# Kernel tuning notes

Measured on AMD Instinct MI355X. Metric: run time of the kernel, lower is better.

## Reference

```python
import jax, jax.numpy as jnp
import numpy as np

B, T, INP, E, H, N = 16, 256, 1536, 512, 8, 16
D = E // H            # 64, must equal default dim_head for to_out shapes to work
SCALE = D ** -0.5
EPS = 1e-5


def _ln(x, g, b):
    m = x.mean(-1, keepdims=True)
    v = ((x - m) ** 2).mean(-1, keepdims=True)
    return (x - m) * jax.lax.rsqrt(v + EPS) * g + b


def _attend(q, k, v, Wo, bo):
    # q,k,v: [bt, h, n, d]. NOTE: attend is LogSoftmax, not Softmax (faithful).
    dots = jnp.einsum('bhnd,bhmd->bhnm', q, k) * SCALE
    a = jax.nn.log_softmax(dots, axis=-1)
    o = jnp.einsum('bhnm,bhmd->bhnd', a, v)
    o = o.transpose(0, 2, 1, 3).reshape(o.shape[0], N, E)  # b n (h d)
    return o @ Wo + bo


def _self_attn(x, Wqkv, Wo, bo):
    # x is already LayerNormed (PreNorm); residual adds the normed x (faithful).
    qkv = x @ Wqkv  # [bt, n, 3E]
    q, k, v = jnp.split(qkv, 3, axis=-1)
    hd = lambda t: t.reshape(t.shape[0], N, H, D).transpose(0, 2, 1, 3)
    return _attend(hd(q), hd(k), hd(v), Wo, bo) + x


def _ff(x, W1, b1, W2, b2):
    # x already LayerNormed; residual adds normed x (faithful to PreNorm+FF).
    return jax.nn.gelu(x @ W1 + b1, approximate=False) @ W2 + b2 + x


def setup_inputs() -> dict:
    key = jax.random.key(0)
    ks = iter(jax.random.split(key, 64))
    nrm = lambda shape, s=0.02: jax.random.normal(next(ks), shape, jnp.float32) * s
    inp = {
        'features': jax.random.normal(next(ks), (B, T, INP), jnp.float32),
        'targets_array': jax.random.randint(next(ks), (B, T), 0, N, jnp.int64),
        'emb': nrm((N, E), 1.0),
        'Wf': nrm((INP, 2 * E * N)), 'bf': jnp.zeros((2 * E * N,), jnp.float32),
        # layer 0: Attention (tuple path: only to_out used)
        'att0_Wo': nrm((E, E)), 'att0_bo': jnp.zeros((E,), jnp.float32),
        'Wm': nrm((E, 1)), 'bm': jnp.zeros((1,), jnp.float32),
    }
    for i in range(3):
        inp[f'ff{i}_g'] = jnp.ones((E,), jnp.float32)
        inp[f'ff{i}_b'] = jnp.zeros((E,), jnp.float32)
        inp[f'ff{i}_W1'] = nrm((E, 2 * E)); inp[f'ff{i}_b1'] = jnp.zeros((2 * E,), jnp.float32)
        inp[f'ff{i}_W2'] = nrm((2 * E, E)); inp[f'ff{i}_b2'] = jnp.zeros((E,), jnp.float32)
    for i in (1, 2):
        inp[f'att{i}_g'] = jnp.ones((E,), jnp.float32)
        inp[f'att{i}_b'] = jnp.zeros((E,), jnp.float32)
        inp[f'att{i}_Wqkv'] = nrm((E, 3 * E))
        inp[f'att{i}_Wo'] = nrm((E, E)); inp[f'att{i}_bo'] = jnp.zeros((E,), jnp.float32)
    return inp


def reference(features, targets_array, emb, Wf, bf, att0_Wo, att0_bo, Wm, bm,
              ff0_g, ff0_b, ff0_W1, ff0_b1, ff0_W2, ff0_b2,
              ff1_g, ff1_b, ff1_W1, ff1_b1, ff1_W2, ff1_b2,
              ff2_g, ff2_b, ff2_W1, ff2_b1, ff2_W2, ff2_b2,
              att1_g, att1_b, att1_Wqkv, att1_Wo, att1_bo,
              att2_g, att2_b, att2_Wqkv, att2_Wo, att2_bo):
    f = features.reshape(-1, INP)                 # [BT, INP]
    t = targets_array.reshape(-1)                 # [BT]
    kv = f @ Wf + bf                              # [BT, 2*E*N]
    k_, v_ = jnp.split(kv, 2, axis=-1)
    nhd = lambda x: x.reshape(-1, N, H, D).transpose(0, 2, 1, 3)  # b (n h d) -> b h n d
    k, v = nhd(k_), nhd(v_)
    q = emb[t].reshape(-1, H, 1, D)               # b h d -> b h 1 d
    q = jnp.broadcast_to(q, (q.shape[0], H, N, D))
    # layer stack: Attn(tuple), PreNorm(FF), PreNorm(Attn), PreNorm(FF), PreNorm(Attn), PreNorm(FF)
    x = _attend(q, k, v, att0_Wo, att0_bo)        # [BT, N, E]
    x = _ff(_ln(x, ff0_g, ff0_b), ff0_W1, ff0_b1, ff0_W2, ff0_b2)
    x = _self_attn(_ln(x, att1_g, att1_b), att1_Wqkv, att1_Wo, att1_bo)
    x = _ff(_ln(x, ff1_g, ff1_b), ff1_W1, ff1_b1, ff1_W2, ff1_b2)
    x = _self_attn(_ln(x, att2_g, att2_b), att2_Wqkv, att2_Wo, att2_bo)
    x = _ff(_ln(x, ff2_g, ff2_b), ff2_W1, ff2_b1, ff2_W2, ff2_b2)
    out = x.mean(axis=1)                          # mean over targets -> [BT, E]
    out = out.reshape(B, T, E)
    mean = out @ Wm + bm                          # [B, T, 1]
    return mean
```

## Files before the change

kernel.cpp:

```cpp
#include <hip/hip_runtime.h>
#include <math.h>

#define BTOT 4096
#define INP  1536
#define EDIM 512
#define NTOK 16
#define KVW  16384
#define ENW  8192
#define FFH  1024
#define NDOT 2048

typedef __attribute__((ext_vector_type(8))) __bf16 bf16x8;
typedef __attribute__((ext_vector_type(4))) float f32x4;

__device__ __forceinline__ ushort f2bf(float f) {
    union { float f; unsigned u; } v; v.f = f;
    unsigned r = v.u + 0x7fffu + ((v.u >> 16) & 1u);
    return (ushort)(r >> 16);
}
__device__ __forceinline__ float bf2f(ushort h) {
    union { unsigned u; float f; } v; v.u = ((unsigned)h) << 16;
    return v.f;
}

__device__ __forceinline__ void transpose_body(
    const float* in, int ld, int c0, int R, ushort* out,
    int bx, int by, int tid)
{
    __shared__ float t[64][65];
    const int bc = bx * 64 + c0;
    const int br = by * 64;
#pragma unroll
    for (int it = 0; it < 16; ++it) {
        int idx = tid + it * 256;
        int r = idx >> 6, c = idx & 63;
        t[r][c] = in[(size_t)(br + r) * ld + bc + c];
    }
    __syncthreads();
    const int C0 = bx * 64;
#pragma unroll
    for (int it = 0; it < 4; ++it) {
        int idx = tid + it * 256;
        int cc = idx >> 4, rp = idx & 15;
        uint2 w2;
        w2.x = f2bf(t[4 * rp + 0][cc]) | ((unsigned)f2bf(t[4 * rp + 1][cc]) << 16);
        w2.y = f2bf(t[4 * rp + 2][cc]) | ((unsigned)f2bf(t[4 * rp + 3][cc]) << 16);
        *reinterpret_cast<uint2*>(out + (size_t)(C0 + cc) * R + br + 4 * rp) = w2;
    }
}

__global__ __launch_bounds__(256) void transpose_bf16_k(
    const float* __restrict__ in, int ld, int c0, int R,
    ushort* __restrict__ out)
{
    transpose_body(in, ld, c0, R, out, blockIdx.x, blockIdx.y, threadIdx.x);
}

struct TJob { const float* in; ushort* out; int ld, c0, R, gbx, gby; };
struct TJobs { TJob j[9]; };

__global__ __launch_bounds__(256) void transpose_batch_k(TJobs jobs)
{
    TJob jb = jobs.j[blockIdx.z];
    if ((int)blockIdx.x >= jb.gbx || (int)blockIdx.y >= jb.gby) return;
    transpose_body(jb.in, jb.ld, jb.c0, jb.R, jb.out,
                   blockIdx.x, blockIdx.y, threadIdx.x);
}

__global__ __launch_bounds__(256) void conv_bf16_k(
    const float* __restrict__ in, ushort* __restrict__ out, int n8)
{
    int i = blockIdx.x * 256 + threadIdx.x;
    if (i >= n8) return;
    const float4* p = reinterpret_cast<const float4*>(in) + 2 * (size_t)i;
    float4 a = p[0], b = p[1];
    uint4 o;
    o.x = f2bf(a.x) | ((unsigned)f2bf(a.y) << 16);
    o.y = f2bf(a.z) | ((unsigned)f2bf(a.w) << 16);
    o.z = f2bf(b.x) | ((unsigned)f2bf(b.y) << 16);
    o.w = f2bf(b.z) | ((unsigned)f2bf(b.w) << 16);
    reinterpret_cast<uint4*>(out)[i] = o;
}

__global__ __launch_bounds__(256) void conv_wv_k(
    const float* __restrict__ s0, const float* __restrict__ s1,
    ushort* __restrict__ d0, ushort* __restrict__ d1)
{
    const float* src = blockIdx.y ? s1 : s0;
    ushort* dst = blockIdx.y ? d1 : d0;
    int idx = blockIdx.x * 256 + threadIdx.x;
    int row = idx >> 6, c8 = (idx & 63) * 8;
    const float4* p = reinterpret_cast<const float4*>(
        src + (size_t)row * (3 * EDIM) + 2 * EDIM + c8);
    float4 a = p[0], b = p[1];
    uint4 o;
    o.x = f2bf(a.x) | ((unsigned)f2bf(a.y) << 16);
    o.y = f2bf(a.z) | ((unsigned)f2bf(a.w) << 16);
    o.z = f2bf(b.x) | ((unsigned)f2bf(b.y) << 16);
    o.w = f2bf(b.z) | ((unsigned)f2bf(b.w) << 16);
    *reinterpret_cast<uint4*>(dst + (size_t)row * EDIM + c8) = o;
}

__global__ __launch_bounds__(256) void gproj_k(
    const float* __restrict__ Wf, const float* __restrict__ bfv,
    const float* __restrict__ emb, ushort* __restrict__ BTg,
    float* __restrict__ C0s)
{
    const int hm = blockIdx.x;
    const int h = hm >> 4, m = hm & 15;
    const int l = threadIdx.x & 63, w = threadIdx.x >> 6;
    const int t = l & 15, isub = l >> 4;
    const int colb = m * 512 + h * 64;
    const int ibase = blockIdx.y * (INP / 8);

    float4 e[16];
#pragma unroll
    for (int q = 0; q < 16; ++q)
        e[q] = *reinterpret_cast<const float4*>(emb + t * EDIM + h * 64 + q * 4);

    const int n = t * 128 + hm;
    for (int i0 = ibase; i0 < ibase + INP / 8; i0 += 16) {
        const int i = i0 + w * 4 + isub;
        const float* wr = Wf + (size_t)i * KVW + colb;
        float acc = 0.f;
#pragma unroll
        for (int q = 0; q < 16; ++q) {
            float4 v4 = *reinterpret_cast<const float4*>(wr + q * 4);
            acc = fmaf(v4.x, e[q].x, fmaf(v4.y, e[q].y,
                  fmaf(v4.z, e[q].z, fmaf(v4.w, e[q].w, acc))));
        }
        BTg[(size_t)n * INP + i] = f2bf(acc);
    }
    if (blockIdx.y == 0 && w == 0 && isub == 0) {
        const float* br = bfv + colb;
        float acc = 0.f;
#pragma unroll
        for (int q = 0; q < 16; ++q) {
            float4 v4 = *reinterpret_cast<const float4*>(br + q * 4);
            acc = fmaf(v4.x, e[q].x, fmaf(v4.y, e[q].y,
                  fmaf(v4.z, e[q].z, fmaf(v4.w, e[q].w, acc))));
        }
        C0s[n] = 0.125f * acc;
    }
}

__global__ __launch_bounds__(256) void sortperm_k(
    const int* __restrict__ targets, int* __restrict__ perm,
    int* __restrict__ boff)
{
    __shared__ int cnt[NTOK], off[NTOK + 1], cur[NTOK];
    const int tid = threadIdx.x;
    if (tid < NTOK) cnt[tid] = 0;
    __syncthreads();
    for (int i = tid; i < BTOT; i += 256) atomicAdd(&cnt[targets[i]], 1);
    __syncthreads();
    if (tid == 0) {
        int s = 0;
        for (int b = 0; b < NTOK; ++b) { off[b] = s; cur[b] = s; s += cnt[b]; }
        off[NTOK] = s;
        for (int b = 0; b <= NTOK; ++b) boff[b] = off[b];
    }
    __syncthreads();
    for (int i = tid; i < BTOT; i += 256) {
        int t = targets[i];
        int p = atomicAdd(&cur[t], 1);
        perm[p] = i;
    }
}

template <int BM, int BN, int WM, int WN, int NW, bool GELU, bool OUTBF>
__global__ __launch_bounds__(NW * 64) void gemm_mfma_k(
    const ushort* __restrict__ A, int lda,
    const ushort* __restrict__ BT, int ldb,
    void* __restrict__ Cp, int ldc, int K,
    const float* __restrict__ bias,
    const float* __restrict__ res, int ldr,
    float scale)
{
    static_assert((BM / WM) * (BN / WN) == NW, "wave grid");
    static_assert(BM % (NW * 8) == 0 && BN % (NW * 8) == 0, "staging");
    constexpr int FM = WM / 16, FN = WN / 16;
    constexpr int IA = BM * 8 / (NW * 64), IB = BN * 8 / (NW * 64);
    constexpr int RA = BM / NW, RB = BN / NW;

    __shared__ bf16x8 As[BM][8];
    __shared__ bf16x8 Bs[BN][8];
    const int tid = threadIdx.x;
    const int l   = tid & 63;
    const int w   = tid >> 6;
    const int wm  = w / (BN / WN), wn = w % (BN / WN);
    const int brow = blockIdx.y * BM, bcol = blockIdx.x * BN;

    const int lr = l >> 3;
    const int ls = (l & 7) ^ lr;
    const ushort* Ab = A  + (size_t)(brow + w * RA + lr) * lda + ls * 8;
    const ushort* Bb = BT + (size_t)(bcol + w * RB + lr) * ldb + ls * 8;

    f32x4 acc[FM][FN];
#pragma unroll
    for (int i = 0; i < FM; ++i)
#pragma unroll
        for (int j = 0; j < FN; ++j) acc[i][j] = (f32x4)0.f;

    for (int k0 = 0; k0 < K; k0 += 64) {
#pragma unroll
        for (int i = 0; i < IA; ++i)
            __builtin_amdgcn_global_load_lds(
                (const __attribute__((address_space(1))) void*)(Ab + (size_t)(i * 8) * lda + k0),
                (__attribute__((address_space(3))) void*)&As[w * RA + i * 8][0],
                16, 0, 0);
#pragma unroll
        for (int i = 0; i < IB; ++i)
            __builtin_amdgcn_global_load_lds(
                (const __attribute__((address_space(1))) void*)(Bb + (size_t)(i * 8) * ldb + k0),
                (__attribute__((address_space(3))) void*)&Bs[w * RB + i * 8][0],
                16, 0, 0);
        __syncthreads();
#pragma unroll
        for (int kh = 0; kh < 2; ++kh) {
            const int slot = (kh * 4 + (l >> 4)) ^ (l & 7);
            bf16x8 af[FM], bfr[FN];
#pragma unroll
            for (int mt = 0; mt < FM; ++mt)
                af[mt] = As[wm * WM + mt * 16 + (l & 15)][slot];
#pragma unroll
            for (int nt = 0; nt < FN; ++nt)
                bfr[nt] = Bs[wn * WN + nt * 16 + (l & 15)][slot];
#pragma unroll
            for (int mt = 0; mt < FM; ++mt)
#pragma unroll
                for (int nt = 0; nt < FN; ++nt)
                    acc[mt][nt] = __builtin_amdgcn_mfma_f32_16x16x32_bf16(
                        af[mt], bfr[nt], acc[mt][nt], 0, 0, 0);
        }
        __syncthreads();
    }

    const int cr = (l >> 4) * 4, cc = l & 15;
#pragma unroll
    for (int mt = 0; mt < FM; ++mt) {
#pragma unroll
        for (int nt = 0; nt < FN; ++nt) {
            const int gc = bcol + wn * WN + nt * 16 + cc;
            const float bv = bias ? bias[gc] : 0.f;
#pragma unroll
            for (int r = 0; r < 4; ++r) {
                const size_t gr = (size_t)brow + wm * WM + mt * 16 + cr + r;
                float v = acc[mt][nt][r] * scale + bv;
                if (GELU) v = 0.5f * v * (1.f + erff(v * 0.70710678118654752f));
                if (res) v += res[gr * ldr + gc];
                if (OUTBF) ((ushort*)Cp)[gr * ldc + gc] = f2bf(v);
                else       ((float*)Cp)[gr * ldc + gc]  = v;
            }
        }
    }
}

__global__ __launch_bounds__(256) void gemm_dots_k(
    const ushort* __restrict__ A,
    const ushort* __restrict__ BT,
    const int* __restrict__ perm, const int* __restrict__ boff,
    const float* __restrict__ C0s, float* __restrict__ Csel)
{
    const int bucket = blockIdx.y;
    const int off = boff[bucket], end = boff[bucket + 1];
    const int tile = blockIdx.x;
    if (tile * 128 >= end - off) return;

    __shared__ bf16x8 As[128][8];
    __shared__ bf16x8 Bs[128][8];
    const int tid = threadIdx.x;
    const int l = tid & 63, w = tid >> 6;
    const int wm = w >> 1, wn = w & 1;
    const int lr = l >> 3;
    const int ls = (l & 7) ^ lr;

    int rowidx[4];
#pragma unroll
    for (int i = 0; i < 4; ++i) {
        int rg = off + tile * 128 + w * 32 + lr + i * 8;
        rowidx[i] = perm[rg < end ? rg : off];
    }
    const ushort* Bb = BT + (size_t)(bucket * 128 + w * 32 + lr) * INP + ls * 8;

    f32x4 acc[4][4];
#pragma unroll
    for (int i = 0; i < 4; ++i)
#pragma unroll
        for (int j = 0; j < 4; ++j) acc[i][j] = (f32x4)0.f;

    for (int k0 = 0; k0 < INP; k0 += 64) {
#pragma unroll
        for (int i = 0; i < 4; ++i)
            __builtin_amdgcn_global_load_lds(
                (const __attribute__((address_space(1))) void*)(
                    A + (size_t)rowidx[i] * INP + ls * 8 + k0),
                (__attribute__((address_space(3))) void*)&As[w * 32 + i * 8][0],
                16, 0, 0);
#pragma unroll
        for (int i = 0; i < 4; ++i)
            __builtin_amdgcn_global_load_lds(
                (const __attribute__((address_space(1))) void*)(
                    Bb + (size_t)(i * 8) * INP + k0),
                (__attribute__((address_space(3))) void*)&Bs[w * 32 + i * 8][0],
                16, 0, 0);
        __syncthreads();
#pragma unroll
        for (int kh = 0; kh < 2; ++kh) {
            const int slot = (kh * 4 + (l >> 4)) ^ (l & 7);
            bf16x8 af[4], bfr[4];
#pragma unroll
            for (int mt = 0; mt < 4; ++mt)
                af[mt] = As[wm * 64 + mt * 16 + (l & 15)][slot];
#pragma unroll
            for (int nt = 0; nt < 4; ++nt)
                bfr[nt] = Bs[wn * 64 + nt * 16 + (l & 15)][slot];
#pragma unroll
            for (int mt = 0; mt < 4; ++mt)
#pragma unroll
                for (int nt = 0; nt < 4; ++nt)
                    acc[mt][nt] = __builtin_amdgcn_mfma_f32_16x16x32_bf16(
                        af[mt], bfr[nt], acc[mt][nt], 0, 0, 0);
        }
        __syncthreads();
    }

    const int cr = (l >> 4) * 4, cc = l & 15;
#pragma unroll
    for (int mt = 0; mt < 4; ++mt) {
#pragma unroll
        for (int nt = 0; nt < 4; ++nt) {
            const int gc = wn * 64 + nt * 16 + cc;
            const float bv = C0s[bucket * 128 + gc];
#pragma unroll
            for (int r = 0; r < 4; ++r) {
                int rg = off + tile * 128 + wm * 64 + mt * 16 + cr + r;
                int orow = perm[rg < end ? rg : off];
                Csel[(size_t)orow * 128 + gc] = acc[mt][nt][r] * 0.125f + bv;
            }
        }
    }
}

__global__ __launch_bounds__(512) void attend0_k(
    const float* __restrict__ dots, const ushort* __restrict__ vb,
    ushort* __restrict__ o)
{
    const int bt = blockIdx.x;
    const int l  = threadIdx.x & 63;
    const int h  = threadIdx.x >> 6;
    const int dg = l & 7, mg = l >> 3;

    const float* dp = dots + (size_t)bt * 128 + h * 16;
    float dts[2] = {dp[mg], dp[8 + mg]};

    float mx = fmaxf(dts[0], dts[1]);
#pragma unroll
    for (int off = 8; off < 64; off <<= 1) mx = fmaxf(mx, __shfl_xor(mx, off, 64));
    float e = expf(dts[0] - mx) + expf(dts[1] - mx);
#pragma unroll
    for (int off = 8; off < 64; off <<= 1) e += __shfl_xor(e, off, 64);
    const float lse = mx + logf(e);
    const float a0 = dts[0] - lse, a1 = dts[1] - lse;

    const ushort* base = vb + (size_t)bt * ENW + h * 64 + dg * 8;
    uint4 v0 = *reinterpret_cast<const uint4*>(base + (size_t)mg * EDIM);
    uint4 v1 = *reinterpret_cast<const uint4*>(base + (size_t)(8 + mg) * EDIM);
    const ushort* u0 = reinterpret_cast<const ushort*>(&v0);
    const ushort* u1 = reinterpret_cast<const ushort*>(&v1);
    float acc[8];
#pragma unroll
    for (int j = 0; j < 8; ++j)
        acc[j] = a0 * bf2f(u0[j]) + a1 * bf2f(u1[j]);
#pragma unroll
    for (int off = 8; off < 64; off <<= 1)
#pragma unroll
        for (int j = 0; j < 8; ++j) acc[j] += __shfl_xor(acc[j], off, 64);

    if (mg == 0) {
        uint4 pk;
        pk.x = f2bf(acc[0]) | ((unsigned)f2bf(acc[1]) << 16);
        pk.y = f2bf(acc[2]) | ((unsigned)f2bf(acc[3]) << 16);
        pk.z = f2bf(acc[4]) | ((unsigned)f2bf(acc[5]) << 16);
        pk.w = f2bf(acc[6]) | ((unsigned)f2bf(acc[7]) << 16);
        *reinterpret_cast<uint4*>(o + (size_t)bt * EDIM + h * 64 + dg * 8) = pk;
    }
}

__global__ __launch_bounds__(256) void ln_k(
    const float* __restrict__ x, const float* __restrict__ g,
    const float* __restrict__ b, float* __restrict__ y,
    ushort* __restrict__ yb)
{
    const int row = blockIdx.x * 4 + (threadIdx.x >> 6);
    const int lane = threadIdx.x & 63;
    const float* xr = x + (size_t)row * EDIM + lane * 8;
    float4 a0 = *reinterpret_cast<const float4*>(xr);
    float4 a1 = *reinterpret_cast<const float4*>(xr + 4);
    float v[8] = {a0.x, a0.y, a0.z, a0.w, a1.x, a1.y, a1.z, a1.w};

    float s = 0.f;
#pragma unroll
    for (int j = 0; j < 8; ++j) s += v[j];
#pragma unroll
    for (int off = 32; off; off >>= 1) s += __shfl_xor(s, off, 64);
    const float m = s * (1.f / 512.f);

    float q = 0.f;
#pragma unroll
    for (int j = 0; j < 8; ++j) { float d = v[j] - m; q = fmaf(d, d, q); }
#pragma unroll
    for (int off = 32; off; off >>= 1) q += __shfl_xor(q, off, 64);
    const float inv = rsqrtf(q * (1.f / 512.f) + 1e-5f);

    const int c = lane * 8;
    float4 g0 = *reinterpret_cast<const float4*>(g + c);
    float4 g1 = *reinterpret_cast<const float4*>(g + c + 4);
    float4 b0 = *reinterpret_cast<const float4*>(b + c);
    float4 b1 = *reinterpret_cast<const float4*>(b + c + 4);
    float gg[8] = {g0.x, g0.y, g0.z, g0.w, g1.x, g1.y, g1.z, g1.w};
    float bb[8] = {b0.x, b0.y, b0.z, b0.w, b1.x, b1.y, b1.z, b1.w};
    float out[8];
#pragma unroll
    for (int j = 0; j < 8; ++j) out[j] = (v[j] - m) * inv * gg[j] + bb[j];
    float* yr = y + (size_t)row * EDIM + c;
    *reinterpret_cast<float4*>(yr) = make_float4(out[0], out[1], out[2], out[3]);
    *reinterpret_cast<float4*>(yr + 4) = make_float4(out[4], out[5], out[6], out[7]);
    uint4 p;
    p.x = f2bf(out[0]) | ((unsigned)f2bf(out[1]) << 16);
    p.y = f2bf(out[2]) | ((unsigned)f2bf(out[3]) << 16);
    p.z = f2bf(out[4]) | ((unsigned)f2bf(out[5]) << 16);
    p.w = f2bf(out[6]) | ((unsigned)f2bf(out[7]) << 16);
    *reinterpret_cast<uint4*>(yb + (size_t)row * EDIM + c) = p;
}

__global__ __launch_bounds__(256) void final_k(
    const float* __restrict__ x, const float* __restrict__ Wm,
    const float* __restrict__ bm, float* __restrict__ out)
{
    const int row = blockIdx.x * 4 + (threadIdx.x >> 6);
    const int lane = threadIdx.x & 63;
    const float* xr = x + (size_t)row * EDIM + lane * 8;
    const float* wr = Wm + lane * 8;
    float s = 0.f;
#pragma unroll
    for (int j = 0; j < 8; ++j) s = fmaf(xr[j], wr[j], s);
#pragma unroll
    for (int off = 32; off; off >>= 1) s += __shfl_xor(s, off, 64);
    if (lane == 0) out[row] = s + bm[0];
}

extern "C" void kernel_launch(void* const* d_in, const int* in_sizes, int n_in,
                              void* d_out, int out_size, void* d_ws, size_t ws_size,
                              hipStream_t stream)
{
    (void)in_sizes; (void)n_in; (void)out_size;
    const float* features = (const float*)d_in[0];
    const int*   targets  = (const int*)d_in[1];
    const float* emb      = (const float*)d_in[2];
    const float* Wf       = (const float*)d_in[3];
    const float* bfv      = (const float*)d_in[4];
    const float* a0Wo     = (const float*)d_in[5];
    const float* a0bo     = (const float*)d_in[6];
    const float* Wm       = (const float*)d_in[7];
    const float* bm       = (const float*)d_in[8];
    const float *ffg[3], *ffb[3], *W1[3], *b1[3], *W2[3], *b2[3];
    for (int i = 0; i < 3; ++i) {
        ffg[i] = (const float*)d_in[9 + 6 * i];
        ffb[i] = (const float*)d_in[10 + 6 * i];
        W1[i]  = (const float*)d_in[11 + 6 * i];
        b1[i]  = (const float*)d_in[12 + 6 * i];
        W2[i]  = (const float*)d_in[13 + 6 * i];
        b2[i]  = (const float*)d_in[14 + 6 * i];
    }
    const float *ag[2], *abp[2], *aWqkv[2], *aWo[2], *abo[2];
    for (int i = 0; i < 2; ++i) {
        ag[i]    = (const float*)d_in[27 + 5 * i];
        abp[i]   = (const float*)d_in[28 + 5 * i];
        aWqkv[i] = (const float*)d_in[29 + 5 * i];
        aWo[i]   = (const float*)d_in[30 + 5 * i];
        abo[i]   = (const float*)d_in[31 + 5 * i];
    }

    char* wsc = (char*)d_ws;
    auto alloc = [&](size_t bytes) { char* p = wsc; wsc += bytes; return p; };
    ushort* WfvT  = (ushort*)alloc((size_t)ENW * INP * 2);
    ushort* BTg   = (ushort*)alloc((size_t)NDOT * INP * 2);
    float*  C0s   = (float*) alloc((size_t)NDOT * 4);
    float*  dsel  = (float*) alloc((size_t)BTOT * 128 * 4);
    int*    perm  = (int*)   alloc((size_t)BTOT * 4);
    int*    boff  = (int*)   alloc(32 * 4);
    ushort* a0WoT = (ushort*)alloc((size_t)EDIM * EDIM * 2);
    ushort *W1T[3], *W2T[3], *WoT[2], *Wv_bf[2], *WcombT[2];
    for (int i = 0; i < 3; ++i) {
        W1T[i] = (ushort*)alloc((size_t)FFH * EDIM * 2);
        W2T[i] = (ushort*)alloc((size_t)EDIM * FFH * 2);
    }
    for (int i = 0; i < 2; ++i) {
        WoT[i]    = (ushort*)alloc((size_t)EDIM * EDIM * 2);
        Wv_bf[i]  = (ushort*)alloc((size_t)EDIM * EDIM * 2);
        WcombT[i] = (ushort*)alloc((size_t)EDIM * EDIM * 2);
    }
    ushort* featb = (ushort*)alloc((size_t)BTOT * INP * 2);
    ushort* o_b   = (ushort*)alloc((size_t)BTOT * EDIM * 2);
    float*  x     = (float*) alloc((size_t)BTOT * EDIM * 4);
    float*  xln   = (float*) alloc((size_t)BTOT * EDIM * 4);
    ushort* xlnb  = (ushort*)alloc((size_t)BTOT * EDIM * 2);
    ushort* hb    = (ushort*)alloc((size_t)BTOT * FFH * 2);
    const size_t fixed = (size_t)(wsc - (char*)d_ws);
    int CB = BTOT;
    while (CB > 256 && fixed + (size_t)CB * ENW * 2 > ws_size) CB >>= 1;
    ushort* vb = (ushort*)alloc((size_t)CB * ENW * 2);

    const dim3 blk(256, 1, 1);

    conv_bf16_k<<<(BTOT * INP / 8 + 255) / 256, blk, 0, stream>>>(
        features, featb, BTOT * INP / 8);
    gproj_k<<<dim3(128, 8), blk, 0, stream>>>(Wf, bfv, emb, BTg, C0s);
    sortperm_k<<<1, blk, 0, stream>>>(targets, perm, boff);
    transpose_bf16_k<<<dim3(ENW / 64, INP / 64), blk, 0, stream>>>(
        Wf, KVW, ENW, INP, WfvT);

    TJobs tj;
    tj.j[0] = {a0Wo, a0WoT, EDIM, 0, EDIM, 8, 8};
    for (int i = 0; i < 3; ++i) {
        tj.j[1 + 2 * i] = {W1[i], W1T[i], FFH, 0, EDIM, 16, 8};
        tj.j[2 + 2 * i] = {W2[i], W2T[i], EDIM, 0, FFH, 8, 16};
    }
    tj.j[7] = {aWo[0], WoT[0], EDIM, 0, EDIM, 8, 8};
    tj.j[8] = {aWo[1], WoT[1], EDIM, 0, EDIM, 8, 8};
    transpose_batch_k<<<dim3(16, 16, 9), blk, 0, stream>>>(tj);

    conv_wv_k<<<dim3(128, 2), blk, 0, stream>>>(aWqkv[0], aWqkv[1],
                                                Wv_bf[0], Wv_bf[1]);

    const float CATT = -44.36141955583650f;
    for (int i = 0; i < 2; ++i)
        gemm_mfma_k<64, 128, 32, 64, 4, false, true>
            <<<dim3(EDIM / 128, EDIM / 64), blk, 0, stream>>>(
            WoT[i], EDIM, Wv_bf[i], EDIM, WcombT[i], EDIM, EDIM,
            nullptr, nullptr, 0, CATT);

    gemm_dots_k<<<dim3(32, 16), blk, 0, stream>>>(featb, BTg, perm, boff,
                                                  C0s, dsel);
    for (int c0 = 0; c0 < BTOT; c0 += CB) {
        gemm_mfma_k<128, 128, 64, 64, 4, false, true>
            <<<dim3(ENW / 128, CB / 128), blk, 0, stream>>>(
            featb + (size_t)c0 * INP, INP, WfvT, INP, vb, ENW, INP,
            bfv + ENW, nullptr, 0, 1.f);
        attend0_k<<<CB, 512, 0, stream>>>(dsel + (size_t)c0 * 128, vb,
                                          o_b + (size_t)c0 * EDIM);
    }
    gemm_mfma_k<64, 128, 32, 64, 4, false, false>
        <<<dim3(EDIM / 128, BTOT / 64), blk, 0, stream>>>(
        o_b, EDIM, a0WoT, EDIM, x, EDIM, EDIM, a0bo, nullptr, 0, 1.f);

    auto ln = [&](const float* g, const float* b) {
        ln_k<<<BTOT / 4, blk, 0, stream>>>(x, g, b, xln, xlnb);
    };
    auto ff = [&](int i) {
        ln(ffg[i], ffb[i]);
        gemm_mfma_k<64, 128, 32, 64, 4, true, true>
            <<<dim3(FFH / 128, BTOT / 64), blk, 0, stream>>>(
            xlnb, EDIM, W1T[i], EDIM, hb, FFH, EDIM, b1[i], nullptr, 0, 1.f);
        gemm_mfma_k<64, 128, 32, 64, 4, false, false>
            <<<dim3(EDIM / 128, BTOT / 64), blk, 0, stream>>>(
            hb, FFH, W2T[i], FFH, x, EDIM, FFH, b2[i], xln, EDIM, 1.f);
    };
    auto attn = [&](int i) {
        ln(ag[i], abp[i]);
        gemm_mfma_k<64, 128, 32, 64, 4, false, false>
            <<<dim3(EDIM / 128, BTOT / 64), blk, 0, stream>>>(
            xlnb, EDIM, WcombT[i], EDIM, x, EDIM, EDIM, abo[i], xln, EDIM, 1.f);
    };

    ff(0);
    attn(0);
    ff(1);
    attn(1);
    ff(2);

    final_k<<<BTOT / 4, blk, 0, stream>>>(x, Wm, bm, (float*)d_out);
}
```

Measured before the change: 493.7 us.

## Fuse V projection with layer-0 attention weighting and move log-softmax into dots epilogue

The big V projection GEMM now writes no 4096x8192 bf16 intermediate. The Wf value columns are transposed into a permuted layout so each 128-column tile holds all 16 tokens for a few head dims. The new GEMM epilogue then multiplies by the log-softmax weights and reduces across tokens with shuffles, writing the attention output directly. Log-softmax moves into the dots GEMM epilogue, and sortperm is folded into the gproj launch as an extra block row. This removes a large HBM round trip and several launches, at the cost of a more complex epilogue and a single-buffered custom GEMM.

```diff
diff --git a/kernel.cpp b/kernel.cpp
--- a/kernel.cpp
+++ b/kernel.cpp
@@ -49,13 +49,6 @@
     }
 }
 
-__global__ __launch_bounds__(256) void transpose_bf16_k(
-    const float* __restrict__ in, int ld, int c0, int R,
-    ushort* __restrict__ out)
-{
-    transpose_body(in, ld, c0, R, out, blockIdx.x, blockIdx.y, threadIdx.x);
-}
-
 struct TJob { const float* in; ushort* out; int ld, c0, R, gbx, gby; };
 struct TJobs { TJob j[9]; };
 
@@ -65,6 +58,35 @@
     if ((int)blockIdx.x >= jb.gbx || (int)blockIdx.y >= jb.gby) return;
     transpose_body(jb.in, jb.ld, jb.c0, jb.R, jb.out,
                    blockIdx.x, blockIdx.y, threadIdx.x);
+}
+
+__global__ __launch_bounds__(256) void transpose_wfvp_k(
+    const float* __restrict__ in, ushort* __restrict__ out)
+{
+    __shared__ float t[64][65];
+    const int tid = threadIdx.x;
+    const int bc = blockIdx.x * 64 + ENW;
+    const int br = blockIdx.y * 64;
+#pragma unroll
+    for (int it = 0; it < 16; ++it) {
+        int idx = tid + it * 256;
+        int r = idx >> 6, c = idx & 63;
+        t[r][c] = in[(size_t)(br + r) * KVW + bc + c];
+    }
+    __syncthreads();
+    const int C0 = blockIdx.x * 64;
+#pragma unroll
+    for (int it = 0; it < 4; ++it) {
+        int idx = tid + it * 256;
+        int cc = idx >> 4, rp = idx & 15;
+        const int n = C0 + cc;
+        const int m = n >> 9, h = (n >> 6) & 7, d8 = (n >> 3) & 7, dl = n & 7;
+        const int np = h * 1024 + d8 * 128 + dl * 16 + m;
+        uint2 w2;
+        w2.x = f2bf(t[4 * rp + 0][cc]) | ((unsigned)f2bf(t[4 * rp + 1][cc]) << 16);
+        w2.y = f2bf(t[4 * rp + 2][cc]) | ((unsigned)f2bf(t[4 * rp + 3][cc]) << 16);
+        *reinterpret_cast<uint2*>(out + (size_t)np * INP + br + 4 * rp) = w2;
+    }
 }
 
 __global__ __launch_bounds__(256) void conv_bf16_k(
@@ -104,8 +126,32 @@
 __global__ __launch_bounds__(256) void gproj_k(
     const float* __restrict__ Wf, const float* __restrict__ bfv,
     const float* __restrict__ emb, ushort* __restrict__ BTg,
-    float* __restrict__ C0s)
-{
+    float* __restrict__ C0s, const int* __restrict__ targets,
+    int* __restrict__ perm, int* __restrict__ boff)
+{
+    if (blockIdx.y == 8) {
+        if (blockIdx.x != 0) return;
+        __shared__ int cnt[NTOK], off_s[NTOK], cur[NTOK];
+        const int tid = threadIdx.x;
+        if (tid < NTOK) cnt[tid] = 0;
+        __syncthreads();
+        for (int i = tid; i < BTOT; i += 256) atomicAdd(&cnt[targets[i]], 1);
+        __syncthreads();
+        if (tid == 0) {
+            int s = 0;
+            for (int b = 0; b < NTOK; ++b) { off_s[b] = s; cur[b] = s; s += cnt[b]; }
+            for (int b = 0; b < NTOK; ++b) boff[b] = off_s[b];
+            boff[NTOK] = s;
+        }
+        __syncthreads();
+        for (int i = tid; i < BTOT; i += 256) {
+            int t = targets[i];
+            int p = atomicAdd(&cur[t], 1);
+            perm[p] = i;
+        }
+        return;
+    }
+
     const int hm = blockIdx.x;
     const int h = hm >> 4, m = hm & 15;
     const int l = threadIdx.x & 63, w = threadIdx.x >> 6;
@@ -141,30 +187,6 @@
                   fmaf(v4.z, e[q].z, fmaf(v4.w, e[q].w, acc))));
         }
         C0s[n] = 0.125f * acc;
-    }
-}
-
-__global__ __launch_bounds__(256) void sortperm_k(
-    const int* __restrict__ targets, int* __restrict__ perm,
-    int* __restrict__ boff)
-{
-    __shared__ int cnt[NTOK], off[NTOK + 1], cur[NTOK];
-    const int tid = threadIdx.x;
-    if (tid < NTOK) cnt[tid] = 0;
-    __syncthreads();
-    for (int i = tid; i < BTOT; i += 256) atomicAdd(&cnt[targets[i]], 1);
-    __syncthreads();
-    if (tid == 0) {
-        int s = 0;
-        for (int b = 0; b < NTOK; ++b) { off[b] = s; cur[b] = s; s += cnt[b]; }
-        off[NTOK] = s;
-        for (int b = 0; b <= NTOK; ++b) boff[b] = off[b];
-    }
-    __syncthreads();
-    for (int i = tid; i < BTOT; i += 256) {
-        int t = targets[i];
-        int p = atomicAdd(&cur[t], 1);
-        perm[p] = i;
     }
 }
 
@@ -334,56 +356,107 @@
             const float bv = C0s[bucket * 128 + gc];
 #pragma unroll
             for (int r = 0; r < 4; ++r) {
+                float val = acc[mt][nt][r] * 0.125f + bv;
+                float mx = val;
+                mx = fmaxf(mx, __shfl_xor(mx, 1, 64));
+                mx = fmaxf(mx, __shfl_xor(mx, 2, 64));
+                mx = fmaxf(mx, __shfl_xor(mx, 4, 64));
+                mx = fmaxf(mx, __shfl_xor(mx, 8, 64));
+                float e = expf(val - mx);
+                e += __shfl_xor(e, 1, 64);
+                e += __shfl_xor(e, 2, 64);
+                e += __shfl_xor(e, 4, 64);
+                e += __shfl_xor(e, 8, 64);
+                const float lse = mx + logf(e);
                 int rg = off + tile * 128 + wm * 64 + mt * 16 + cr + r;
                 int orow = perm[rg < end ? rg : off];
-                Csel[(size_t)orow * 128 + gc] = acc[mt][nt][r] * 0.125f + bv;
+                Csel[(size_t)orow * 128 + gc] = val - lse;
             }
         }
     }
 }
 
-__global__ __launch_bounds__(512) void attend0_k(
-    const float* __restrict__ dots, const ushort* __restrict__ vb,
+__global__ __launch_bounds__(256) void gemm_vo_k(
+    const ushort* __restrict__ A,
+    const ushort* __restrict__ BT,
+    const float* __restrict__ biasv,
+    const float* __restrict__ dsel,
     ushort* __restrict__ o)
 {
-    const int bt = blockIdx.x;
-    const int l  = threadIdx.x & 63;
-    const int h  = threadIdx.x >> 6;
-    const int dg = l & 7, mg = l >> 3;
-
-    const float* dp = dots + (size_t)bt * 128 + h * 16;
-    float dts[2] = {dp[mg], dp[8 + mg]};
-
-    float mx = fmaxf(dts[0], dts[1]);
-#pragma unroll
-    for (int off = 8; off < 64; off <<= 1) mx = fmaxf(mx, __shfl_xor(mx, off, 64));
-    float e = expf(dts[0] - mx) + expf(dts[1] - mx);
-#pragma unroll
-    for (int off = 8; off < 64; off <<= 1) e += __shfl_xor(e, off, 64);
-    const float lse = mx + logf(e);
-    const float a0 = dts[0] - lse, a1 = dts[1] - lse;
-
-    const ushort* base = vb + (size_t)bt * ENW + h * 64 + dg * 8;
-    uint4 v0 = *reinterpret_cast<const uint4*>(base + (size_t)mg * EDIM);
-    uint4 v1 = *reinterpret_cast<const uint4*>(base + (size_t)(8 + mg) * EDIM);
-    const ushort* u0 = reinterpret_cast<const ushort*>(&v0);
-    const ushort* u1 = reinterpret_cast<const ushort*>(&v1);
-    float acc[8];
-#pragma unroll
-    for (int j = 0; j < 8; ++j)
-        acc[j] = a0 * bf2f(u0[j]) + a1 * bf2f(u1[j]);
-#pragma unroll
-    for (int off = 8; off < 64; off <<= 1)
-#pragma unroll
-        for (int j = 0; j < 8; ++j) acc[j] += __shfl_xor(acc[j], off, 64);
-
-    if (mg == 0) {
-        uint4 pk;
-        pk.x = f2bf(acc[0]) | ((unsigned)f2bf(acc[1]) << 16);
-        pk.y = f2bf(acc[2]) | ((unsigned)f2bf(acc[3]) << 16);
-        pk.z = f2bf(acc[4]) | ((unsigned)f2bf(acc[5]) << 16);
-        pk.w = f2bf(acc[6]) | ((unsigned)f2bf(acc[7]) << 16);
-        *reinterpret_cast<uint4*>(o + (size_t)bt * EDIM + h * 64 + dg * 8) = pk;
+    __shared__ bf16x8 As[128][8];
+    __shared__ bf16x8 Bs[128][8];
+    const int tid = threadIdx.x;
+    const int l = tid & 63, w = tid >> 6;
+    const int wm = w >> 1, wn = w & 1;
+    const int brow = blockIdx.y * 128, bcol = blockIdx.x * 128;
+    const int h = blockIdx.x >> 3, d8 = blockIdx.x & 7;
+    const int lr = l >> 3;
+    const int ls = (l & 7) ^ lr;
+    const ushort* Ab = A  + (size_t)(brow + w * 32 + lr) * INP + ls * 8;
+    const ushort* Bb = BT + (size_t)(bcol + w * 32 + lr) * INP + ls * 8;
+
+    f32x4 acc[4][4];
+#pragma unroll
+    for (int i = 0; i < 4; ++i)
+#pragma unroll
+        for (int j = 0; j < 4; ++j) acc[i][j] = (f32x4)0.f;
+
+    for (int k0 = 0; k0 < INP; k0 += 64) {
+#pragma unroll
+        for (int i = 0; i < 4; ++i)
+            __builtin_amdgcn_global_load_lds(
+                (const __attribute__((address_space(1))) void*)(Ab + (size_t)(i * 8) * INP + k0),
+                (__attribute__((address_space(3))) void*)&As[w * 32 + i * 8][0],
+                16, 0, 0);
+#pragma unroll
+        for (int i = 0; i < 4; ++i)
+            __builtin_amdgcn_global_load_lds(
+                (const __attribute__((address_space(1))) void*)(Bb + (size_t)(i * 8) * INP + k0),
+                (__attribute__((address_space(3))) void*)&Bs[w * 32 + i * 8][0],
+                16, 0, 0);
+        __syncthreads();
+#pragma unroll
+        for (int kh = 0; kh < 2; ++kh) {
+            const int slot = (kh * 4 + (l >> 4)) ^ (l & 7);
+            bf16x8 af[4], bfr[4];
+#pragma unroll
+            for (int mt = 0; mt < 4; ++mt)
+                af[mt] = As[wm * 64 + mt * 16 + (l & 15)][slot];
+#pragma unroll
+            for (int nt = 0; nt < 4; ++nt)
+                bfr[nt] = Bs[wn * 64 + nt * 16 + (l & 15)][slot];
+#pragma unroll
+            for (int mt = 0; mt < 4; ++mt)
+#pragma unroll
+                for (int nt = 0; nt < 4; ++nt)
+                    acc[mt][nt] = __builtin_amdgcn_mfma_f32_16x16x32_bf16(
+                        af[mt], bfr[nt], acc[mt][nt], 0, 0, 0);
+        }
+        __syncthreads();
+    }
+
+    const int cr = (l >> 4) * 4, cc = l & 15;
+    float bv[4];
+#pragma unroll
+    for (int nt = 0; nt < 4; ++nt)
+        bv[nt] = biasv[cc * 512 + h * 64 + d8 * 8 + wn * 4 + nt];
+#pragma unroll
+    for (int mt = 0; mt < 4; ++mt) {
+#pragma unroll
+        for (int r = 0; r < 4; ++r) {
+            const int gr = brow + wm * 64 + mt * 16 + cr + r;
+            const float wgt = dsel[(size_t)gr * 128 + h * 16 + cc];
+#pragma unroll
+            for (int nt = 0; nt < 4; ++nt) {
+                float s = (acc[mt][nt][r] + bv[nt]) * wgt;
+                s += __shfl_xor(s, 1, 64);
+                s += __shfl_xor(s, 2, 64);
+                s += __shfl_xor(s, 4, 64);
+                s += __shfl_xor(s, 8, 64);
+                if (cc == 0)
+                    o[(size_t)gr * EDIM + h * 64 + d8 * 8 + wn * 4 + nt] = f2bf(s);
+            }
+        }
     }
 }
 
@@ -454,7 +527,7 @@
                               void* d_out, int out_size, void* d_ws, size_t ws_size,
                               hipStream_t stream)
 {
-    (void)in_sizes; (void)n_in; (void)out_size;
+    (void)in_sizes; (void)n_in; (void)out_size; (void)ws_size;
     const float* features = (const float*)d_in[0];
     const int*   targets  = (const int*)d_in[1];
     const float* emb      = (const float*)d_in[2];
@@ -484,7 +557,7 @@
 
     char* wsc = (char*)d_ws;
     auto alloc = [&](size_t bytes) { char* p = wsc; wsc += bytes; return p; };
-    ushort* WfvT  = (ushort*)alloc((size_t)ENW * INP * 2);
+    ushort* WfvTp = (ushort*)alloc((size_t)ENW * INP * 2);
     ushort* BTg   = (ushort*)alloc((size_t)NDOT * INP * 2);
     float*  C0s   = (float*) alloc((size_t)NDOT * 4);
     float*  dsel  = (float*) alloc((size_t)BTOT * 128 * 4);
@@ -507,19 +580,14 @@
     float*  xln   = (float*) alloc((size_t)BTOT * EDIM * 4);
     ushort* xlnb  = (ushort*)alloc((size_t)BTOT * EDIM * 2);
     ushort* hb    = (ushort*)alloc((size_t)BTOT * FFH * 2);
-    const size_t fixed = (size_t)(wsc - (char*)d_ws);
-    int CB = BTOT;
-    while (CB > 256 && fixed + (size_t)CB * ENW * 2 > ws_size) CB >>= 1;
-    ushort* vb = (ushort*)alloc((size_t)CB * ENW * 2);
 
     const dim3 blk(256, 1, 1);
 
     conv_bf16_k<<<(BTOT * INP / 8 + 255) / 256, blk, 0, stream>>>(
         features, featb, BTOT * INP / 8);
-    gproj_k<<<dim3(128, 8), blk, 0, stream>>>(Wf, bfv, emb, BTg, C0s);
-    sortperm_k<<<1, blk, 0, stream>>>(targets, perm, boff);
-    transpose_bf16_k<<<dim3(ENW / 64, INP / 64), blk, 0, stream>>>(
-        Wf, KVW, ENW, INP, WfvT);
+    gproj_k<<<dim3(128, 9), blk, 0, stream>>>(Wf, bfv, emb, BTg, C0s,
+                                              targets, perm, boff);
+    transpose_wfvp_k<<<dim3(ENW / 64, INP / 64), blk, 0, stream>>>(Wf, WfvTp);
 
     TJobs tj;
     tj.j[0] = {a0Wo, a0WoT, EDIM, 0, EDIM, 8, 8};
@@ -543,14 +611,8 @@
 
     gemm_dots_k<<<dim3(32, 16), blk, 0, stream>>>(featb, BTg, perm, boff,
                                                   C0s, dsel);
-    for (int c0 = 0; c0 < BTOT; c0 += CB) {
-        gemm_mfma_k<128, 128, 64, 64, 4, false, true>
-            <<<dim3(ENW / 128, CB / 128), blk, 0, stream>>>(
-            featb + (size_t)c0 * INP, INP, WfvT, INP, vb, ENW, INP,
-            bfv + ENW, nullptr, 0, 1.f);
-        attend0_k<<<CB, 512, 0, stream>>>(dsel + (size_t)c0 * 128, vb,
-                                          o_b + (size_t)c0 * EDIM);
-    }
+    gemm_vo_k<<<dim3(ENW / 128, BTOT / 128), blk, 0, stream>>>(
+        featb, WfvTp, bfv + ENW, dsel, o_b);
     gemm_mfma_k<64, 128, 32, 64, 4, false, false>
         <<<dim3(EDIM / 128, BTOT / 64), blk, 0, stream>>>(
         o_b, EDIM, a0WoT, EDIM, x, EDIM, EDIM, a0bo, nullptr, 0, 1.f);
```

After: 507.0 us. 2.7% more time.
